# Performance work log

Measured on AMD Instinct MI355X. Metric: run time of the kernel, lower is better.

Reference implementation:

```python
import jax, jax.numpy as jnp
import numpy as np

N_NODES = 100000
N_EDGES = 600000
D_FEAT = 128
D_DOT = 4


def setup_inputs() -> dict:
    key = jax.random.key(0)
    k1, k2, k3, k4, k5 = jax.random.split(key, 5)
    n = jax.random.normal(k1, (N_NODES, D_FEAT), dtype=jnp.float32)
    e = jax.random.normal(k2, (N_EDGES, D_FEAT), dtype=jnp.float32)
    # xavier_uniform for Linear(D_FEAT, D_DOT); bias filled with 0
    limit = float(np.sqrt(6.0 / (D_FEAT + D_DOT)))
    W = jax.random.uniform(k3, (D_DOT, D_FEAT), dtype=jnp.float32, minval=-limit, maxval=limit)
    b = jnp.zeros((D_DOT,), dtype=jnp.float32)
    src_idx = jax.random.randint(k4, (N_EDGES,), 0, N_NODES, dtype=jnp.int64)
    dst_idx = jax.random.randint(k5, (N_EDGES,), 0, N_NODES, dtype=jnp.int64)
    return {"n": n, "e": e, "W": W, "b": b, "src_idx": src_idx, "dst_idx": dst_idx}


def reference(n, e, W, b, src_idx, dst_idx):
    # gather per-edge src/dst node features: [E, D]
    src = n[src_idx]
    dst = n[dst_idx]
    # include_edge_features=True: mean of node and edge features
    src = (src + e) * 0.5
    dst = (dst + e) * 0.5
    # tiny linear projection to dot_product_dim=4: [E, 4]
    hs = src @ W.T + b
    hd = dst @ W.T + b
    # per-edge dot product (bmm of [E,1,4] x [E,4,1] -> [E,1]) then sigmoid
    score = jax.nn.sigmoid(jnp.sum(hs * hd, axis=-1, keepdims=True))
    return score
```

## Files before the change

### kernel.cpp

```cpp
#include <hip/hip_runtime.h>
#include <math.h>

#define D_FEAT 128
#define D_DOT  4


typedef float vfloat4 __attribute__((ext_vector_type(4)));

__device__ __forceinline__ float dot4v(const vfloat4 a, const float4 b) {
    return a.x * b.x + a.y * b.y + a.z * b.z + a.w * b.w;
}

__device__ __forceinline__ vfloat4 ntload4(const float* p) {
    return __builtin_nontemporal_load(reinterpret_cast<const vfloat4*>(p));
}

template <int CTRL>
__device__ __forceinline__ float dpp_add(float x) {
    union { float f; int i; } u, v;
    u.f = x;
    v.i = __builtin_amdgcn_update_dpp(u.i, u.i, CTRL, 0xF, 0xF, true);
    return x + v.f;
}

__device__ __forceinline__ float row_reduce16(float x) {
    x = dpp_add<0x128>(x);
    x = dpp_add<0x124>(x);
    x = dpp_add<0x122>(x);
    x = dpp_add<0x121>(x);
    return x;
}

#define U 4

__global__ __launch_bounds__(256, 4) void node_proj_kernel(
    const float* __restrict__ n,
    const float* __restrict__ W,
    float* __restrict__ pn,
    int n_nodes)
{
    const int t    = threadIdx.x;
    const int lane = t & 63;
    const int sub  = lane & 15;
    const int g    = lane >> 4;
    const int wave = t >> 6;
    const int base = blockIdx.x * (U * 16) + wave * (U * 4);
    const int last = n_nodes - 1;

    int r[U], c[U];
#pragma unroll
    for (int i = 0; i < U; ++i) {
        r[i] = base + i * 4 + g;
        c[i] = r[i] > last ? last : r[i];
    }

    vfloat4 xl[U], xh[U];
#pragma unroll
    for (int i = 0; i < U; ++i) {
        xl[i] = ntload4(&n[(size_t)c[i] * D_FEAT + sub * 4]);
        xh[i] = ntload4(&n[(size_t)c[i] * D_FEAT + 64 + sub * 4]);
    }

    const float4* W4 = reinterpret_cast<const float4*>(W);
    float4 wlo[D_DOT], whi[D_DOT];
#pragma unroll
    for (int k = 0; k < D_DOT; ++k) {
        wlo[k] = W4[k * 32 + sub];
        whi[k] = W4[k * 32 + sub + 16];
    }

    float a[U][D_DOT];
#pragma unroll
    for (int i = 0; i < U; ++i)
#pragma unroll
        for (int k = 0; k < D_DOT; ++k)
            a[i][k] = dot4v(xl[i], wlo[k]) + dot4v(xh[i], whi[k]);

#pragma unroll
    for (int i = 0; i < U; ++i)
#pragma unroll
        for (int k = 0; k < D_DOT; ++k)
            a[i][k] = row_reduce16(a[i][k]);

#pragma unroll
    for (int i = 0; i < U; ++i)
        if (sub == 0 && r[i] < n_nodes)
            reinterpret_cast<float4*>(pn)[r[i]] =
                make_float4(0.5f * a[i][0], 0.5f * a[i][1],
                            0.5f * a[i][2], 0.5f * a[i][3]);
}

__global__ __launch_bounds__(256, 3) void edge_score_kernel(
    const float* __restrict__ e,
    const float* __restrict__ W,
    const float* __restrict__ bias,
    const float* __restrict__ pn,
    const int* __restrict__ src_idx,
    const int* __restrict__ dst_idx,
    float* __restrict__ out,
    int n_edges)
{
    const int t    = threadIdx.x;
    const int lane = t & 63;
    const int sub  = lane & 15;
    const int g    = lane >> 4;
    const int wave = t >> 6;
    const int base = blockIdx.x * (U * 16) + wave * (U * 4);
    const int last = n_edges - 1;

    int r[U], c[U];
#pragma unroll
    for (int i = 0; i < U; ++i) {
        r[i] = base + i * 4 + g;
        c[i] = r[i] > last ? last : r[i];
    }

    int sI[U], dI[U];
#pragma unroll
    for (int i = 0; i < U; ++i) { sI[i] = src_idx[c[i]]; dI[i] = dst_idx[c[i]]; }

    vfloat4 xl[U], xh[U];
#pragma unroll
    for (int i = 0; i < U; ++i) {
        xl[i] = ntload4(&e[(size_t)c[i] * D_FEAT + sub * 4]);
        xh[i] = ntload4(&e[(size_t)c[i] * D_FEAT + 64 + sub * 4]);
    }

    const float4* pn4 = reinterpret_cast<const float4*>(pn);
    float4 ps[U], pd[U];
#pragma unroll
    for (int i = 0; i < U; ++i) { ps[i] = pn4[sI[i]]; pd[i] = pn4[dI[i]]; }

    const float4* W4 = reinterpret_cast<const float4*>(W);
    float4 wlo[D_DOT], whi[D_DOT];
#pragma unroll
    for (int k = 0; k < D_DOT; ++k) {
        wlo[k] = W4[k * 32 + sub];
        whi[k] = W4[k * 32 + sub + 16];
    }
    const float b0 = bias[0], b1 = bias[1], b2 = bias[2], b3 = bias[3];

    float a[U][D_DOT];
#pragma unroll
    for (int i = 0; i < U; ++i)
#pragma unroll
        for (int k = 0; k < D_DOT; ++k)
            a[i][k] = dot4v(xl[i], wlo[k]) + dot4v(xh[i], whi[k]);

#pragma unroll
    for (int i = 0; i < U; ++i)
#pragma unroll
        for (int k = 0; k < D_DOT; ++k)
            a[i][k] = row_reduce16(a[i][k]);

#pragma unroll
    for (int i = 0; i < U; ++i) {
        const float u0 = 0.5f * a[i][0] + b0, u1 = 0.5f * a[i][1] + b1;
        const float u2 = 0.5f * a[i][2] + b2, u3 = 0.5f * a[i][3] + b3;
        const float dot = (ps[i].x + u0) * (pd[i].x + u0)
                        + (ps[i].y + u1) * (pd[i].y + u1)
                        + (ps[i].z + u2) * (pd[i].z + u2)
                        + (ps[i].w + u3) * (pd[i].w + u3);
        if (sub == 0 && r[i] < n_edges)
            out[r[i]] = 1.0f / (1.0f + __expf(-dot));
    }
}

extern "C" void kernel_launch(void* const* d_in, const int* in_sizes, int n_in,
                              void* d_out, int out_size, void* d_ws, size_t ws_size,
                              hipStream_t stream) {
    const float* n    = (const float*)d_in[0];
    const float* e    = (const float*)d_in[1];
    const float* W    = (const float*)d_in[2];
    const float* bias = (const float*)d_in[3];
    const int*   src  = (const int*)d_in[4];
    const int*   dst  = (const int*)d_in[5];
    float* out = (float*)d_out;

    const int n_nodes = in_sizes[0] / D_FEAT;
    const int n_edges = in_sizes[1] / D_FEAT;

    float* pn = (float*)d_ws;

    const int nblk = (n_nodes + 63) / 64;
    const int eblk = (n_edges + 63) / 64;
    node_proj_kernel<<<nblk, 256, 0, stream>>>(n, W, pn, n_nodes);
    edge_score_kernel<<<eblk, 256, 0, stream>>>(e, W, bias, pn, src, dst, out, n_edges);
}
```

Measured before the change: 73.18 us.

## Merge node and edge projections into one launch, move gather to epilogue

```diff
diff --git a/kernel.cpp b/kernel.cpp
--- a/kernel.cpp
+++ b/kernel.cpp
@@ -3,6 +3,7 @@
 
 #define D_FEAT 128
 #define D_DOT  4
+#define U      4
 
 
 typedef float vfloat4 __attribute__((ext_vector_type(4)));
@@ -31,21 +32,18 @@
     return x;
 }
 
-#define U 4
-
-__global__ __launch_bounds__(256, 4) void node_proj_kernel(
-    const float* __restrict__ n,
-    const float* __restrict__ W,
-    float* __restrict__ pn,
-    int n_nodes)
+__device__ __forceinline__ void project_rows(
+    const float* __restrict__ src, float4* __restrict__ dst4,
+    const float* __restrict__ W, int n_rows, int block_i,
+    float ab0, float ab1, float ab2, float ab3)
 {
     const int t    = threadIdx.x;
     const int lane = t & 63;
     const int sub  = lane & 15;
     const int g    = lane >> 4;
     const int wave = t >> 6;
-    const int base = blockIdx.x * (U * 16) + wave * (U * 4);
-    const int last = n_nodes - 1;
+    const int base = block_i * (U * 16) + wave * (U * 4);
+    const int last = n_rows - 1;
 
     int r[U], c[U];
 #pragma unroll
@@ -57,8 +55,8 @@
     vfloat4 xl[U], xh[U];
 #pragma unroll
     for (int i = 0; i < U; ++i) {
-        xl[i] = ntload4(&n[(size_t)c[i] * D_FEAT + sub * 4]);
-        xh[i] = ntload4(&n[(size_t)c[i] * D_FEAT + 64 + sub * 4]);
+        xl[i] = ntload4(&src[(size_t)c[i] * D_FEAT + sub * 4]);
+        xh[i] = ntload4(&src[(size_t)c[i] * D_FEAT + 64 + sub * 4]);
     }
 
     const float4* W4 = reinterpret_cast<const float4*>(W);
@@ -84,86 +82,52 @@
 
 #pragma unroll
     for (int i = 0; i < U; ++i)
-        if (sub == 0 && r[i] < n_nodes)
-            reinterpret_cast<float4*>(pn)[r[i]] =
-                make_float4(0.5f * a[i][0], 0.5f * a[i][1],
-                            0.5f * a[i][2], 0.5f * a[i][3]);
+        if (sub == 0 && r[i] < n_rows)
+            dst4[r[i]] = make_float4(0.5f * a[i][0] + ab0, 0.5f * a[i][1] + ab1,
+                                     0.5f * a[i][2] + ab2, 0.5f * a[i][3] + ab3);
 }
 
-__global__ __launch_bounds__(256, 3) void edge_score_kernel(
+__global__ __launch_bounds__(256, 4) void stream_proj_kernel(
     const float* __restrict__ e,
+    const float* __restrict__ n,
     const float* __restrict__ W,
     const float* __restrict__ bias,
+    float* __restrict__ q,
+    float* __restrict__ pn,
+    int n_edges, int n_nodes, int eblk)
+{
+    if ((int)blockIdx.x < eblk) {
+        const float b0 = bias[0], b1 = bias[1], b2 = bias[2], b3 = bias[3];
+        project_rows(e, reinterpret_cast<float4*>(q), W, n_edges, blockIdx.x,
+                     b0, b1, b2, b3);
+    } else {
+        project_rows(n, reinterpret_cast<float4*>(pn), W, n_nodes,
+                     blockIdx.x - eblk, 0.f, 0.f, 0.f, 0.f);
+    }
+}
+
+__global__ __launch_bounds__(256, 8) void edge_epilogue_kernel(
+    const float* __restrict__ q,
     const float* __restrict__ pn,
     const int* __restrict__ src_idx,
     const int* __restrict__ dst_idx,
     float* __restrict__ out,
     int n_edges)
 {
-    const int t    = threadIdx.x;
-    const int lane = t & 63;
-    const int sub  = lane & 15;
-    const int g    = lane >> 4;
-    const int wave = t >> 6;
-    const int base = blockIdx.x * (U * 16) + wave * (U * 4);
-    const int last = n_edges - 1;
+    const int tid = blockIdx.x * 256 + threadIdx.x;
+    if (tid >= n_edges) return;
 
-    int r[U], c[U];
-#pragma unroll
-    for (int i = 0; i < U; ++i) {
-        r[i] = base + i * 4 + g;
-        c[i] = r[i] > last ? last : r[i];
-    }
+    const int s = src_idx[tid];
+    const int d = dst_idx[tid];
+    const float4 qe = reinterpret_cast<const float4*>(q)[tid];
+    const float4 ps = reinterpret_cast<const float4*>(pn)[s];
+    const float4 pd = reinterpret_cast<const float4*>(pn)[d];
 
-    int sI[U], dI[U];
-#pragma unroll
-    for (int i = 0; i < U; ++i) { sI[i] = src_idx[c[i]]; dI[i] = dst_idx[c[i]]; }
-
-    vfloat4 xl[U], xh[U];
-#pragma unroll
-    for (int i = 0; i < U; ++i) {
-        xl[i] = ntload4(&e[(size_t)c[i] * D_FEAT + sub * 4]);
-        xh[i] = ntload4(&e[(size_t)c[i] * D_FEAT + 64 + sub * 4]);
-    }
-
-    const float4* pn4 = reinterpret_cast<const float4*>(pn);
-    float4 ps[U], pd[U];
-#pragma unroll
-    for (int i = 0; i < U; ++i) { ps[i] = pn4[sI[i]]; pd[i] = pn4[dI[i]]; }
-
-    const float4* W4 = reinterpret_cast<const float4*>(W);
-    float4 wlo[D_DOT], whi[D_DOT];
-#pragma unroll
-    for (int k = 0; k < D_DOT; ++k) {
-        wlo[k] = W4[k * 32 + sub];
-        whi[k] = W4[k * 32 + sub + 16];
-    }
-    const float b0 = bias[0], b1 = bias[1], b2 = bias[2], b3 = bias[3];
-
-    float a[U][D_DOT];
-#pragma unroll
-    for (int i = 0; i < U; ++i)
-#pragma unroll
-        for (int k = 0; k < D_DOT; ++k)
-            a[i][k] = dot4v(xl[i], wlo[k]) + dot4v(xh[i], whi[k]);
-
-#pragma unroll
-    for (int i = 0; i < U; ++i)
-#pragma unroll
-        for (int k = 0; k < D_DOT; ++k)
-            a[i][k] = row_reduce16(a[i][k]);
-
-#pragma unroll
-    for (int i = 0; i < U; ++i) {
-        const float u0 = 0.5f * a[i][0] + b0, u1 = 0.5f * a[i][1] + b1;
-        const float u2 = 0.5f * a[i][2] + b2, u3 = 0.5f * a[i][3] + b3;
-        const float dot = (ps[i].x + u0) * (pd[i].x + u0)
-                        + (ps[i].y + u1) * (pd[i].y + u1)
-                        + (ps[i].z + u2) * (pd[i].z + u2)
-                        + (ps[i].w + u3) * (pd[i].w + u3);
-        if (sub == 0 && r[i] < n_edges)
-            out[r[i]] = 1.0f / (1.0f + __expf(-dot));
-    }
+    const float dot = (ps.x + qe.x) * (pd.x + qe.x)
+                    + (ps.y + qe.y) * (pd.y + qe.y)
+                    + (ps.z + qe.z) * (pd.z + qe.z)
+                    + (ps.w + qe.w) * (pd.w + qe.w);
+    out[tid] = 1.0f / (1.0f + __expf(-dot));
 }
 
 extern "C" void kernel_launch(void* const* d_in, const int* in_sizes, int n_in,
@@ -181,9 +145,13 @@
     const int n_edges = in_sizes[1] / D_FEAT;
 
     float* pn = (float*)d_ws;
+    float* q  = pn + (size_t)n_nodes * D_DOT;
 
+    const int eblk = (n_edges + 63) / 64;
     const int nblk = (n_nodes + 63) / 64;
-    const int eblk = (n_edges + 63) / 64;
-    node_proj_kernel<<<nblk, 256, 0, stream>>>(n, W, pn, n_nodes);
-    edge_score_kernel<<<eblk, 256, 0, stream>>>(e, W, bias, pn, src, dst, out, n_edges);
+    stream_proj_kernel<<<eblk + nblk, 256, 0, stream>>>(
+        e, n, W, bias, q, pn, n_edges, n_nodes, eblk);
+
+    const int pblk = (n_edges + 255) / 256;
+    edge_epilogue_kernel<<<pblk, 256, 0, stream>>>(q, pn, src, dst, out, n_edges);
 }
```

Result: faster. 70.80 us (-3.3%).
